# Kernel optimization log

Hardware: AMD Instinct MI355X
Metric: run time of the kernel (lower is better)

## Reference

```python
import jax, jax.numpy as jnp
import numpy as np

SEQ = 2048
D_MODEL = 1024
N_HEADS = 16
TOP_K = 64
Q_LR = 128
KV_LR = 128
ROPE_DIM = 32
V_DIM = 64
IDX_DIM = 64
# Mamba2 indexer block: expand=1, headdim=32, d_state=64, d_conv=4
D_INNER = D_MODEL
M_HD = 32
M_NH = D_INNER // M_HD  # 32 ssm heads
M_DS = 64
M_DC = 4
CONV_CH = D_INNER + 2 * M_DS  # 1152
IN_DIM = 2 * D_INNER + 2 * M_DS + M_NH  # 2208


def _silu(x):
    return x * jax.nn.sigmoid(x)


def _mamba2(x, in_w, conv_w, conv_b, dt_bias, A_log, D, norm_w, out_w):
    # Minimal Mamba2 (SSD) recurrent forward: in_proj -> causal depthwise conv
    # on (x, B, C) -> selective scan with scalar-per-head A -> gated RMSNorm -> out_proj.
    L = x.shape[0]
    zxbcdt = x @ in_w.T  # [L, IN_DIM]
    z = zxbcdt[:, :D_INNER]
    xBC = zxbcdt[:, D_INNER:D_INNER + CONV_CH]
    dt = zxbcdt[:, -M_NH:]
    # causal depthwise conv1d, kernel M_DC
    xp = jnp.pad(xBC, ((M_DC - 1, 0), (0, 0)))
    conv = conv_b
    for k in range(M_DC):
        conv = conv + xp[k:k + L] * conv_w[:, k]
    xBC = _silu(conv)
    xs = xBC[:, :D_INNER].reshape(L, M_NH, M_HD)          # [L,h,p]
    B = xBC[:, D_INNER:D_INNER + M_DS]                     # [L,n]
    C = xBC[:, D_INNER + M_DS:]                            # [L,n]
    dt = jax.nn.softplus(dt + dt_bias)                     # [L,h]
    dA = jnp.exp(dt * (-jnp.exp(A_log)))                   # [L,h]
    dBx = jnp.einsum('lh,lhp,ln->lhpn', dt, xs, B)         # [L,h,p,n]

    def step(h, inp):
        dA_t, dBx_t, C_t = inp
        h = h * dA_t[:, None, None] + dBx_t
        y_t = jnp.einsum('hpn,n->hp', h, C_t)
        return h, y_t

    h0 = jnp.zeros((M_NH, M_HD, M_DS), x.dtype)
    _, y = jax.lax.scan(step, h0, (dA, dBx, C))            # y: [L,h,p]
    y = y + D[:, None] * xs
    y = y.reshape(L, D_INNER) * _silu(z)                   # gated
    y = y * jax.lax.rsqrt(jnp.mean(y * y, axis=-1, keepdims=True) + 1e-5) * norm_w
    return y @ out_w.T


def _make_rope(L):
    inv = 1.0 / (10000.0 ** (jnp.arange(0, ROPE_DIM, 2, dtype=jnp.float32) / ROPE_DIM))
    ang = jnp.arange(L, dtype=jnp.float32)[:, None] * inv  # [L, ROPE/2]
    return jnp.sin(ang), jnp.cos(ang)


def _apply_rope(x, sin, cos):
    # x: [L, H, ROPE_DIM]; rotate-half convention
    x1, x2 = jnp.split(x, 2, axis=-1)
    s = sin[:, None, :]
    c = cos[:, None, :]
    return jnp.concatenate([x1 * c - x2 * s, x1 * s + x2 * c], axis=-1)


def _forward(x, idx_in_w, idx_conv_w, idx_conv_b, idx_dt_bias, idx_A_log, idx_D,
             idx_norm_w, idx_out_w, idx_q_w, idx_k_w, q_down_w, q_up_w, q_rope_w,
             kv_down_w, kv_up_w, k_rope_w, out_w):
    L = x.shape[0]
    # --- Mamba2 indexer scores ---
    x_mamba = _mamba2(x, idx_in_w, idx_conv_w, idx_conv_b, idx_dt_bias,
                      idx_A_log, idx_D, idx_norm_w, idx_out_w)
    q_idx = x_mamba @ idx_q_w.T                            # [L, IDX_DIM]
    k_idx = x @ idx_k_w.T                                  # [L, IDX_DIM]
    scores = (q_idx @ k_idx.T) * (IDX_DIM ** -0.5)         # [L, L]
    mask = jnp.tril(jnp.ones((L, L), dtype=bool))
    scores = jnp.where(mask, scores, -jnp.inf)
    k_val = min(TOP_K, L)
    _, indices = jax.lax.top_k(scores, k_val)              # [L, K]
    # --- MLA low-rank projections ---
    c_q = x @ q_down_w.T                                   # [L, Q_LR]
    q_content = (c_q @ q_up_w.T).reshape(L, N_HEADS, V_DIM)
    q_rope = (c_q @ q_rope_w.T).reshape(L, N_HEADS, ROPE_DIM)
    c_kv = x @ kv_down_w.T                                 # [L, KV_LR]
    kv = c_kv @ kv_up_w.T                                  # [L, 2*H*V]
    k_content_flat, v_flat = jnp.split(kv, 2, axis=-1)
    k_content = k_content_flat.reshape(L, N_HEADS, V_DIM)
    v = v_flat.reshape(L, N_HEADS, V_DIM)
    k_rope_shared = (x @ k_rope_w.T)[:, None, :]           # [L, 1, ROPE]
    sin, cos = _make_rope(L)
    q_rope_rot = _apply_rope(q_rope, sin, cos)
    k_rope_rot = jnp.tile(_apply_rope(k_rope_shared, sin, cos), (1, N_HEADS, 1))
    q_final = jnp.concatenate([q_content, q_rope_rot], axis=-1)  # [L,H,dk]
    k_final = jnp.concatenate([k_content, k_rope_rot], axis=-1)  # [L,H,dk]
    # --- top-k gather sparse attention ---
    k_sparse = k_final[indices]                            # [L,K,H,dk]
    v_sparse = v[indices]                                  # [L,K,H,dv]
    dk = k_final.shape[-1]
    logits = jnp.einsum('lhd,lkhd->lhk', q_final, k_sparse) * (dk ** -0.5)
    w = jax.nn.softmax(logits, axis=-1)
    attn = jnp.einsum('lhk,lkhd->lhd', w, v_sparse).reshape(L, N_HEADS * V_DIM)
    return attn @ out_w.T


def setup_inputs() -> dict:
    key = jax.random.key(0)
    ks = jax.random.split(key, 16)

    def g(k, shape, s=0.02):
        return jax.random.normal(k, shape, jnp.float32) * s

    return {
        "x": jax.random.normal(ks[0], (SEQ, D_MODEL), jnp.float32),
        "idx_in_w": g(ks[1], (IN_DIM, D_MODEL)),
        "idx_conv_w": g(ks[2], (CONV_CH, M_DC), 0.2),
        "idx_conv_b": jnp.zeros((CONV_CH,), jnp.float32),
        "idx_dt_bias": g(ks[3], (M_NH,), 0.1),
        "idx_A_log": jnp.log(jnp.arange(1, M_NH + 1, dtype=jnp.float32)),
        "idx_D": jnp.ones((M_NH,), jnp.float32),
        "idx_norm_w": jnp.ones((D_INNER,), jnp.float32),
        "idx_out_w": g(ks[4], (D_MODEL, D_INNER)),
        "idx_q_w": g(ks[5], (IDX_DIM, D_MODEL)),
        "idx_k_w": g(ks[6], (IDX_DIM, D_MODEL)),
        "q_down_w": g(ks[7], (Q_LR, D_MODEL)),
        "q_up_w": g(ks[8], (N_HEADS * V_DIM, Q_LR)),
        "q_rope_w": g(ks[9], (N_HEADS * ROPE_DIM, Q_LR)),
        "kv_down_w": g(ks[10], (KV_LR, D_MODEL)),
        "kv_up_w": g(ks[11], (2 * N_HEADS * V_DIM, KV_LR)),
        "k_rope_w": g(ks[12], (ROPE_DIM, D_MODEL)),
        "out_w": g(ks[13], (D_MODEL, N_HEADS * V_DIM)),
    }


def reference(x, idx_in_w, idx_conv_w, idx_conv_b, idx_dt_bias, idx_A_log, idx_D,
              idx_norm_w, idx_out_w, idx_q_w, idx_k_w, q_down_w, q_up_w, q_rope_w,
              kv_down_w, kv_up_w, k_rope_w, out_w):
    return _forward(x, idx_in_w, idx_conv_w, idx_conv_b, idx_dt_bias, idx_A_log,
                    idx_D, idx_norm_w, idx_out_w, idx_q_w, idx_k_w, q_down_w,
                    q_up_w, q_rope_w, kv_down_w, kv_up_w, k_rope_w, out_w)
```

## Files before the change

kernel.cpp:

```cpp
#include <hip/hip_runtime.h>
#include <math.h>

constexpr int L      = 2048;
constexpr int NH     = 16;
constexpr int DINNER = 1024;
constexpr int MNH    = 32;
constexpr int CONVCH = 1152;
constexpr int INDIMP = 2304;
constexpr int CHUNK  = 64;
constexpr int NCH    = 32;

using bf16x8 = __attribute__((ext_vector_type(8))) short;
using f32x4  = __attribute__((ext_vector_type(4))) float;

__device__ __forceinline__ f32x4 splat4(float x) { return (f32x4){x, x, x, x}; }

__device__ __forceinline__ unsigned short f2bf(float f) {
  unsigned u = __float_as_uint(f);
  return (unsigned short)((u + 0x7fffu + ((u >> 16) & 1u)) >> 16);
}
__device__ __forceinline__ float bf2f(unsigned short h) {
  return __uint_as_float((unsigned)h << 16);
}

__global__ __launch_bounds__(256) void gemm_f32_v3(
    const float* __restrict__ A, const float* __restrict__ W,
    float* __restrict__ C, int M, int N, int K, int tri) {
  __shared__ float As[16][132];
  __shared__ float Ws[16][132];
  int tid = threadIdx.x;
  int bm = blockIdx.y * 128, bn = blockIdx.x * 128;
  if (tri && bn > bm + 127) return;
  int kper = K / gridDim.z;
  int kb = blockIdx.z * kper, ke = kb + kper;
  int lr = tid >> 1;
  int lh = (tid & 1) * 8;
  int tx = tid & 15, ty = tid >> 4;
  bool wok = (bn + lr < N);
  const float* arow = A + (size_t)(bm + lr) * K + lh;
  const float* wrow = W + (size_t)(bn + lr) * K + lh;
  float4 a0, a1, w0, w1;
  auto gload = [&](int k0) {
    a0 = *(const float4*)(arow + k0);
    a1 = *(const float4*)(arow + k0 + 4);
    w0 = make_float4(0.f, 0.f, 0.f, 0.f); w1 = w0;
    if (wok) {
      w0 = *(const float4*)(wrow + k0);
      w1 = *(const float4*)(wrow + k0 + 4);
    }
  };
  f32x4 acc0[8] = {}, acc1[8] = {};
  gload(kb);
  for (int k0 = kb; k0 < ke; k0 += 16) {
    __syncthreads();
    As[lh+0][lr]=a0.x; As[lh+1][lr]=a0.y; As[lh+2][lr]=a0.z; As[lh+3][lr]=a0.w;
    As[lh+4][lr]=a1.x; As[lh+5][lr]=a1.y; As[lh+6][lr]=a1.z; As[lh+7][lr]=a1.w;
    Ws[lh+0][lr]=w0.x; Ws[lh+1][lr]=w0.y; Ws[lh+2][lr]=w0.z; Ws[lh+3][lr]=w0.w;
    Ws[lh+4][lr]=w1.x; Ws[lh+5][lr]=w1.y; Ws[lh+6][lr]=w1.z; Ws[lh+7][lr]=w1.w;
    __syncthreads();
    if (k0 + 16 < ke) gload(k0 + 16);
#pragma unroll
    for (int kk = 0; kk < 16; ++kk) {
      f32x4 b0 = *(const f32x4*)&Ws[kk][tx * 4];
      f32x4 b1 = *(const f32x4*)&Ws[kk][64 + tx * 4];
      f32x4 al = *(const f32x4*)&As[kk][ty * 8];
      f32x4 ah = *(const f32x4*)&As[kk][ty * 8 + 4];
#pragma unroll
      for (int i = 0; i < 4; ++i) {
        acc0[i]     += splat4(al[i]) * b0;
        acc1[i]     += splat4(al[i]) * b1;
        acc0[i + 4] += splat4(ah[i]) * b0;
        acc1[i + 4] += splat4(ah[i]) * b1;
      }
    }
  }
  bool single = (gridDim.z == 1);
#pragma unroll
  for (int i = 0; i < 8; ++i) {
    int row = bm + ty * 8 + i;
    float* crow = C + (size_t)row * N;
    int c0 = bn + tx * 4, c1 = bn + 64 + tx * 4;
    if (c0 + 3 < N) {
      if (single) *(f32x4*)(crow + c0) = acc0[i];
      else {
        atomicAdd(crow + c0 + 0, acc0[i][0]); atomicAdd(crow + c0 + 1, acc0[i][1]);
        atomicAdd(crow + c0 + 2, acc0[i][2]); atomicAdd(crow + c0 + 3, acc0[i][3]);
      }
    }
    if (c1 + 3 < N) {
      if (single) *(f32x4*)(crow + c1) = acc1[i];
      else {
        atomicAdd(crow + c1 + 0, acc1[i][0]); atomicAdd(crow + c1 + 1, acc1[i][1]);
        atomicAdd(crow + c1 + 2, acc1[i][2]); atomicAdd(crow + c1 + 3, acc1[i][3]);
      }
    }
  }
}

__global__ __launch_bounds__(256) void gemm_f32_dual(
    const float* __restrict__ A0, const float* __restrict__ W0, float* __restrict__ C0,
    const float* __restrict__ A1, const float* __restrict__ W1, float* __restrict__ C1,
    int M, int N, int K, int S) {
  __shared__ float As[16][132];
  __shared__ float Ws[16][132];
  int tid = threadIdx.x;
  int bm = blockIdx.y * 128, bn = blockIdx.x * 128;
  int pair = (int)blockIdx.z >= S;
  int zi = blockIdx.z - pair * S;
  const float* A = pair ? A1 : A0;
  const float* W = pair ? W1 : W0;
  float* C = pair ? C1 : C0;
  int kper = K / S;
  int kb = zi * kper, ke = kb + kper;
  int lr = tid >> 1;
  int lh = (tid & 1) * 8;
  int tx = tid & 15, ty = tid >> 4;
  bool wok = (bn + lr < N);
  const float* arow = A + (size_t)(bm + lr) * K + lh;
  const float* wrow = W + (size_t)(bn + lr) * K + lh;
  float4 a0, a1, w0, w1;
  auto gload = [&](int k0) {
    a0 = *(const float4*)(arow + k0);
    a1 = *(const float4*)(arow + k0 + 4);
    w0 = make_float4(0.f, 0.f, 0.f, 0.f); w1 = w0;
    if (wok) {
      w0 = *(const float4*)(wrow + k0);
      w1 = *(const float4*)(wrow + k0 + 4);
    }
  };
  f32x4 acc0[8] = {}, acc1[8] = {};
  gload(kb);
  for (int k0 = kb; k0 < ke; k0 += 16) {
    __syncthreads();
    As[lh+0][lr]=a0.x; As[lh+1][lr]=a0.y; As[lh+2][lr]=a0.z; As[lh+3][lr]=a0.w;
    As[lh+4][lr]=a1.x; As[lh+5][lr]=a1.y; As[lh+6][lr]=a1.z; As[lh+7][lr]=a1.w;
    Ws[lh+0][lr]=w0.x; Ws[lh+1][lr]=w0.y; Ws[lh+2][lr]=w0.z; Ws[lh+3][lr]=w0.w;
    Ws[lh+4][lr]=w1.x; Ws[lh+5][lr]=w1.y; Ws[lh+6][lr]=w1.z; Ws[lh+7][lr]=w1.w;
    __syncthreads();
    if (k0 + 16 < ke) gload(k0 + 16);
#pragma unroll
    for (int kk = 0; kk < 16; ++kk) {
      f32x4 b0 = *(const f32x4*)&Ws[kk][tx * 4];
      f32x4 b1 = *(const f32x4*)&Ws[kk][64 + tx * 4];
      f32x4 al = *(const f32x4*)&As[kk][ty * 8];
      f32x4 ah = *(const f32x4*)&As[kk][ty * 8 + 4];
#pragma unroll
      for (int i = 0; i < 4; ++i) {
        acc0[i]     += splat4(al[i]) * b0;
        acc1[i]     += splat4(al[i]) * b1;
        acc0[i + 4] += splat4(ah[i]) * b0;
        acc1[i + 4] += splat4(ah[i]) * b1;
      }
    }
  }
#pragma unroll
  for (int i = 0; i < 8; ++i) {
    int row = bm + ty * 8 + i;
    float* crow = C + (size_t)row * N;
    int c0 = bn + tx * 4, c1 = bn + 64 + tx * 4;
    if (c0 + 3 < N) {
      atomicAdd(crow + c0 + 0, acc0[i][0]); atomicAdd(crow + c0 + 1, acc0[i][1]);
      atomicAdd(crow + c0 + 2, acc0[i][2]); atomicAdd(crow + c0 + 3, acc0[i][3]);
    }
    if (c1 + 3 < N) {
      atomicAdd(crow + c1 + 0, acc1[i][0]); atomicAdd(crow + c1 + 1, acc1[i][1]);
      atomicAdd(crow + c1 + 2, acc1[i][2]); atomicAdd(crow + c1 + 3, acc1[i][3]);
    }
  }
}

__global__ __launch_bounds__(256) void gemm_bf16_kernel(
    const unsigned short* __restrict__ A, const unsigned short* __restrict__ W,
    float* __restrict__ C, int M, int N, int K, int lda, int ldb, int ldc) {
  __shared__ unsigned short As[2][128 * 64];
  __shared__ unsigned short Ws[2][128 * 64];
  int tid = threadIdx.x;
  int bx = blockIdx.x, by = blockIdx.y;
  int nxy = gridDim.x * gridDim.y;
  if ((nxy & 7) == 0) {
    int lin = by * gridDim.x + bx;
    int cpx = nxy >> 3;
    int swz = (lin & 7) * cpx + (lin >> 3);
    bx = swz % gridDim.x;
    by = swz / gridDim.x;
  }
  int bm = by * 128, bn = bx * 128;
  int kper = K / gridDim.z;
  int k_begin = blockIdx.z * kper;
  int k_end = k_begin + kper;
  int wv = tid >> 6, lane = tid & 63;
  int wrow = (wv >> 1) * 64, wcol = (wv & 1) * 64;
  int lrow = lane & 15, quad = lane >> 4;

  f32x4 acc[4][4] = {};

  auto stage = [&](int b, int k0) {
#pragma unroll
    for (int it = 0; it < 4; ++it) {
      int s = it * 256 + tid;
      int r = s >> 3;
      int q = (s & 7) ^ (r & 7);
      const unsigned short* ga = A + (size_t)(bm + r) * lda + k0 + q * 8;
      const unsigned short* gw = W + (size_t)(bn + r) * ldb + k0 + q * 8;
      __builtin_amdgcn_global_load_lds((const __attribute__((address_space(1))) void*)ga,
                                       (__attribute__((address_space(3))) void*)&As[b][s * 8], 16, 0, 0);
      __builtin_amdgcn_global_load_lds((const __attribute__((address_space(1))) void*)gw,
                                       (__attribute__((address_space(3))) void*)&Ws[b][s * 8], 16, 0, 0);
    }
  };

  stage(0, k_begin);
  int cur = 0;
  for (int k0 = k_begin; k0 < k_end; k0 += 64) {
    __syncthreads();
    if (k0 + 64 < k_end) stage(cur ^ 1, k0 + 64);
#pragma unroll
    for (int ks = 0; ks < 2; ++ks) {
      bf16x8 af[4], wf[4];
#pragma unroll
      for (int i = 0; i < 4; ++i) {
        int ra = wrow + i * 16 + lrow;
        int qa = (ks * 4 + quad) ^ (ra & 7);
        af[i] = *(const bf16x8*)&As[cur][(ra * 8 + qa) * 8];
        int rw = wcol + i * 16 + lrow;
        int qw = (ks * 4 + quad) ^ (rw & 7);
        wf[i] = *(const bf16x8*)&Ws[cur][(rw * 8 + qw) * 8];
      }
#pragma unroll
      for (int i = 0; i < 4; ++i)
#pragma unroll
        for (int j = 0; j < 4; ++j)
          acc[i][j] = __builtin_amdgcn_mfma_f32_16x16x32_bf16(af[i], wf[j], acc[i][j], 0, 0, 0);
    }
    cur ^= 1;
  }
  bool single = (gridDim.z == 1);
#pragma unroll
  for (int i = 0; i < 4; ++i)
#pragma unroll
    for (int j = 0; j < 4; ++j)
#pragma unroll
      for (int r = 0; r < 4; ++r) {
        int row = bm + wrow + i * 16 + quad * 4 + r;
        int col = bn + wcol + j * 16 + lrow;
        float v = acc[i][j][r];
        if (single) C[(size_t)row * ldc + col] = v;
        else atomicAdd(&C[(size_t)row * ldc + col], v);
      }
}

__global__ __launch_bounds__(512) void gemm_bf16_256_kernel(
    const unsigned short* __restrict__ A, const unsigned short* __restrict__ W,
    float* __restrict__ C, int K, int lda, int ldc) {
  __shared__ unsigned short As[4][256 * 32];
  __shared__ unsigned short Ws[4][256 * 32];
  int tid = threadIdx.x;
  int bx = blockIdx.x, by = blockIdx.y;
  int nxy = gridDim.x * gridDim.y;
  if ((nxy & 7) == 0) {
    int lin = by * gridDim.x + bx;
    int cpx = nxy >> 3;
    int swz = (lin & 7) * cpx + (lin >> 3);
    bx = swz % gridDim.x;
    by = swz / gridDim.x;
  }
  int bm = by * 256, bn = bx * 256;
  int kper = K / gridDim.z;
  int kb = blockIdx.z * kper;
  int U = kper >> 5;
  int wave = tid >> 6, lane = tid & 63;
  int wr = wave >> 2, wc = wave & 3;
  int lrow = lane & 15, quad = lane >> 4;

  f32x4 acc[8][4] = {};

  auto stage = [&](int cell, int u) {
    int k0 = kb + (u << 5);
#pragma unroll
    for (int rd = 0; rd < 2; ++rd) {
      int s = rd * 512 + tid;
      int r = s >> 2;
      int q = (s & 3) ^ ((r >> 1) & 3);
      const unsigned short* ga = A + (size_t)(bm + r) * lda + k0 + q * 8;
      __builtin_amdgcn_global_load_lds((const __attribute__((address_space(1))) void*)ga,
          (__attribute__((address_space(3))) void*)&As[cell][s * 8], 16, 0, 0);
    }
#pragma unroll
    for (int rd = 0; rd < 2; ++rd) {
      int s = rd * 512 + tid;
      int r = s >> 2;
      int q = (s & 3) ^ ((r >> 1) & 3);
      const unsigned short* gw = W + (size_t)(bn + r) * lda + k0 + q * 8;
      __builtin_amdgcn_global_load_lds((const __attribute__((address_space(1))) void*)gw,
          (__attribute__((address_space(3))) void*)&Ws[cell][s * 8], 16, 0, 0);
    }
  };

  auto compute = [&](int cell) {
    bf16x8 af[8], wf[4];
#pragma unroll
    for (int m = 0; m < 8; ++m) {
      int ra = wr * 128 + m * 16 + lrow;
      af[m] = *(const bf16x8*)&As[cell][((ra << 2) + (quad ^ ((ra >> 1) & 3))) * 8];
    }
#pragma unroll
    for (int n = 0; n < 4; ++n) {
      int rw = wc * 64 + n * 16 + lrow;
      wf[n] = *(const bf16x8*)&Ws[cell][((rw << 2) + (quad ^ ((rw >> 1) & 3))) * 8];
    }
    __builtin_amdgcn_s_setprio(1);
#pragma unroll
    for (int m = 0; m < 8; ++m)
#pragma unroll
      for (int n = 0; n < 4; ++n)
        acc[m][n] = __builtin_amdgcn_mfma_f32_16x16x32_bf16(af[m], wf[n], acc[m][n], 0, 0, 0);
    __builtin_amdgcn_s_setprio(0);
  };

  stage(0, 0); stage(1, 1); stage(2, 2);
  for (int u = 0; u + 3 < U; ++u) {
    __builtin_amdgcn_s_barrier();
    asm volatile("" ::: "memory");
    stage((u + 3) & 3, u + 3);
    asm volatile("s_waitcnt vmcnt(12)" ::: "memory");
    __builtin_amdgcn_s_barrier();
    asm volatile("" ::: "memory");
    compute(u & 3);
  }
  for (int u = U - 3; u < U; ++u) {
    __builtin_amdgcn_s_barrier();
    asm volatile("s_waitcnt vmcnt(0)" ::: "memory");
    __builtin_amdgcn_s_barrier();
    asm volatile("" ::: "memory");
    compute(u & 3);
  }

#pragma unroll
  for (int m = 0; m < 8; ++m)
#pragma unroll
    for (int n = 0; n < 4; ++n)
#pragma unroll
      for (int rr = 0; rr < 4; ++rr) {
        int row = bm + wr * 128 + m * 16 + quad * 4 + rr;
        int col = bn + wc * 64 + n * 16 + lrow;
        atomicAdd(&C[(size_t)row * ldc + col], acc[m][n][rr]);
      }
}

__global__ __launch_bounds__(256) void gemm_bf16_dual(
    const unsigned short* __restrict__ A0, const unsigned short* __restrict__ W0,
    float* __restrict__ C0,
    const unsigned short* __restrict__ A1, const unsigned short* __restrict__ W1,
    float* __restrict__ C1,
    int nx0, int ldc0, int ldc1, int K, int ld) {
  __shared__ unsigned short As[2][128 * 64];
  __shared__ unsigned short Ws[2][128 * 64];
  int tid = threadIdx.x;
  int bx = blockIdx.x, by = blockIdx.y;
  int pair = bx >= nx0;
  int bxl = pair ? bx - nx0 : bx;
  const unsigned short* A = pair ? A1 : A0;
  const unsigned short* W = pair ? W1 : W0;
  float* C = pair ? C1 : C0;
  int ldc = pair ? ldc1 : ldc0;
  int bm = by * 128, bn = bxl * 128;
  int wv = tid >> 6, lane = tid & 63;
  int wrow = (wv >> 1) * 64, wcol = (wv & 1) * 64;
  int lrow = lane & 15, quad = lane >> 4;

  f32x4 acc[4][4] = {};

  auto stage = [&](int b, int k0) {
#pragma unroll
    for (int it = 0; it < 4; ++it) {
      int s = it * 256 + tid;
      int r = s >> 3;
      int q = (s & 7) ^ (r & 7);
      const unsigned short* ga = A + (size_t)(bm + r) * ld + k0 + q * 8;
      const unsigned short* gw = W + (size_t)(bn + r) * ld + k0 + q * 8;
      __builtin_amdgcn_global_load_lds((const __attribute__((address_space(1))) void*)ga,
                                       (__attribute__((address_space(3))) void*)&As[b][s * 8], 16, 0, 0);
      __builtin_amdgcn_global_load_lds((const __attribute__((address_space(1))) void*)gw,
                                       (__attribute__((address_space(3))) void*)&Ws[b][s * 8], 16, 0, 0);
    }
  };

  stage(0, 0);
  int cur = 0;
  for (int k0 = 0; k0 < K; k0 += 64) {
    __syncthreads();
    if (k0 + 64 < K) stage(cur ^ 1, k0 + 64);
#pragma unroll
    for (int ks = 0; ks < 2; ++ks) {
      bf16x8 af[4], wf[4];
#pragma unroll
      for (int i = 0; i < 4; ++i) {
        int ra = wrow + i * 16 + lrow;
        int qa = (ks * 4 + quad) ^ (ra & 7);
        af[i] = *(const bf16x8*)&As[cur][(ra * 8 + qa) * 8];
        int rw = wcol + i * 16 + lrow;
        int qw = (ks * 4 + quad) ^ (rw & 7);
        wf[i] = *(const bf16x8*)&Ws[cur][(rw * 8 + qw) * 8];
      }
#pragma unroll
      for (int i = 0; i < 4; ++i)
#pragma unroll
        for (int j = 0; j < 4; ++j)
          acc[i][j] = __builtin_amdgcn_mfma_f32_16x16x32_bf16(af[i], wf[j], acc[i][j], 0, 0, 0);
    }
    cur ^= 1;
  }
#pragma unroll
  for (int i = 0; i < 4; ++i)
#pragma unroll
    for (int j = 0; j < 4; ++j)
#pragma unroll
      for (int r = 0; r < 4; ++r) {
        int row = bm + wrow + i * 16 + quad * 4 + r;
        int col = bn + wcol + j * 16 + lrow;
        C[(size_t)row * ldc + col] = acc[i][j][r];
      }
}

__global__ __launch_bounds__(256) void prep_weights_kernel(
    const float* __restrict__ x, unsigned short* __restrict__ x_trip,
    const float* __restrict__ idx_in_w, unsigned short* __restrict__ w_in_trip,
    const float* __restrict__ q_down_w, const float* __restrict__ kv_down_w,
    const float* __restrict__ k_rope_w, unsigned short* __restrict__ w3down,
    const float* __restrict__ q_up_w, const float* __restrict__ q_rope_w,
    unsigned short* __restrict__ wqups,
    const float* __restrict__ kv_up_w, unsigned short* __restrict__ wkvup,
    const float* __restrict__ idx_out_w, float* __restrict__ out_w_T,
    const float* __restrict__ idx_q_w, float* __restrict__ qwpad,
    float* __restrict__ zxbcdt) {
  __shared__ float tsh[32][33];
  int bid = blockIdx.x;
  if (bid >= 22784) {
    int j = (bid - 22784) * 256 + threadIdx.x;
    zxbcdt[j] = 0.f;
    return;
  }
  if (bid >= 21760) {
    int j = (bid - 21760) * 256 + threadIdx.x;
    qwpad[j] = (j < 65536) ? idx_q_w[j] : 0.f;
    return;
  }
  if (bid >= 20736) {
    int b = bid - 20736;
    int bx = b & 31, by = b >> 5;
    int tx = threadIdx.x & 31, ty8 = threadIdx.x >> 5;
    for (int r = ty8; r < 32; r += 8)
      tsh[r][tx] = idx_out_w[(size_t)(by * 32 + r) * 1024 + bx * 32 + tx];
    __syncthreads();
    for (int r = ty8; r < 32; r += 8)
      out_w_T[(size_t)(bx * 32 + r) * 1024 + by * 32 + tx] = tsh[tx][r];
    return;
  }
  int i = bid * 256 + threadIdx.x;
  if (i < 2097152) {
    float f = x[i];
    unsigned short h = f2bf(f);
    float r1 = f - bf2f(h);
    unsigned short m = f2bf(r1);
    unsigned short l = f2bf(r1 - bf2f(m));
    size_t o = (size_t)i * 6;
    x_trip[o] = h; x_trip[o + 1] = m; x_trip[o + 2] = l;
    x_trip[o + 3] = h; x_trip[o + 4] = m; x_trip[o + 5] = h;
  } else if (i < 4456448) {
    int j = i - 2097152;
    int n = j >> 10, k = j & 1023;
    unsigned short h = 0, m = 0, l = 0;
    if (n < 2208) {
      float f = idx_in_w[(size_t)n * 1024 + k];
      h = f2bf(f);
      float r1 = f - bf2f(h);
      m = f2bf(r1);
      l = f2bf(r1 - bf2f(m));
    }
    size_t o = (size_t)j * 6;
    w_in_trip[o] = h; w_in_trip[o + 1] = h; w_in_trip[o + 2] = h;
    w_in_trip[o + 3] = m; w_in_trip[o + 4] = m; w_in_trip[o + 5] = l;
  } else {
    int j2 = i - 4456448;
    const float* src; unsigned short* dst; int rows, K; size_t obase; int idx;
    if (j2 < 393216) {
      int r = j2 >> 17;
      idx = j2 & 131071;
      K = 1024;
      src = (r == 0) ? q_down_w : (r == 1) ? kv_down_w : k_rope_w;
      rows = (r == 2) ? 32 : 128;
      dst = w3down; obase = (size_t)(r * 131072 + idx) * 3;
    } else if (j2 < 524288) {
      idx = j2 - 393216; K = 128; src = q_up_w; rows = 1024;
      dst = wqups; obase = (size_t)idx * 3;
    } else if (j2 < 589824) {
      idx = j2 - 524288; K = 128; src = q_rope_w; rows = 512;
      dst = wqups; obase = (size_t)393216 + (size_t)idx * 3;
    } else {
      idx = j2 - 589824; K = 128; src = kv_up_w; rows = 2048;
      dst = wkvup; obase = (size_t)idx * 3;
    }
    int n = idx / K, k = idx - n * K;
    unsigned short hi = 0, lo = 0;
    if (n < rows) {
      float f = src[(size_t)n * K + k];
      hi = f2bf(f);
      lo = f2bf(f - bf2f(hi));
    }
    dst[obase] = hi; dst[obase + 1] = hi; dst[obase + 2] = lo;
  }
}

__global__ __launch_bounds__(256) void post_inproj_kernel(
    const float* __restrict__ out_w, unsigned short* __restrict__ w_outp,
    const float* __restrict__ zxbcdt, const float* __restrict__ conv_w,
    const float* __restrict__ conv_b, float* __restrict__ xBC,
    const float* __restrict__ dt_bias, const float* __restrict__ A_log,
    float* __restrict__ dt, float* __restrict__ logdA) {
  int i = blockIdx.x * 256 + threadIdx.x;
  if (i < 1048576) {
    float f = out_w[i];
    unsigned short hi = f2bf(f);
    unsigned short lo = f2bf(f - bf2f(hi));
    size_t o = (size_t)i * 3;
    w_outp[o] = hi; w_outp[o + 1] = hi; w_outp[o + 2] = lo;
  } else if (i < 3407872) {
    int idx = i - 1048576;
    int l = idx / CONVCH, c = idx - l * CONVCH;
    float acc = conv_b[c];
#pragma unroll
    for (int k = 0; k < 4; ++k) {
      int ls = l - 3 + k;
      if (ls >= 0) acc += zxbcdt[(size_t)ls * INDIMP + DINNER + c] * conv_w[c * 4 + k];
    }
    xBC[idx] = acc / (1.f + expf(-acc));
  } else {
    int idx = i - 3407872;
    int l = idx >> 5, h = idx & 31;
    float xv = zxbcdt[(size_t)l * INDIMP + 2176 + h] + dt_bias[h];
    float sp = fmaxf(xv, 0.f) + log1pf(expf(-fabsf(xv)));
    dt[idx] = sp;
    logdA[idx] = sp * -expf(A_log[h]);
  }
}

__global__ __launch_bounds__(256) void conv_augA2_kernel(
    const float* __restrict__ c3, unsigned short* __restrict__ dq,
    unsigned short* __restrict__ dkv) {
  int i = blockIdx.x * 256 + threadIdx.x;
  if (i >= 2048 * 256) return;
  int m = i >> 8, k = i & 255;
  float f = c3[(size_t)m * 384 + k];
  unsigned short hi = f2bf(f);
  unsigned short lo = f2bf(f - bf2f(hi));
  if (k < 128) {
    size_t o = ((size_t)m * 128 + k) * 3;
    dq[o] = hi; dq[o + 1] = lo; dq[o + 2] = hi;
  } else {
    size_t o = ((size_t)m * 128 + (k - 128)) * 3;
    dkv[o] = hi; dkv[o + 1] = lo; dkv[o + 2] = hi;
  }
}

__global__ __launch_bounds__(256) void chunk_G_kernel(
    const float* __restrict__ xBC, float* __restrict__ G,
    const float* __restrict__ logdA, float* __restrict__ lcd) {
  int c = blockIdx.x, tid = threadIdx.x;
  if (c >= NCH) {
    int i = (c - NCH) * 256 + tid;
    int cc = i >> 5, h = i & 31;
    float s = 0.f;
    for (int t = 0; t < CHUNK; ++t) {
      s += logdA[(cc * CHUNK + t) * MNH + h];
      lcd[(size_t)i * CHUNK + t] = s;
    }
    return;
  }
  __shared__ float BsT[64][68];
  __shared__ float Cs[64][65];
  int t = tid >> 2, q = tid & 3;
  const float* row = xBC + (size_t)(c * 64 + t) * CONVCH + DINNER;
#pragma unroll
  for (int j = 0; j < 16; j += 4) {
    float4 b = *(const float4*)(row + q * 16 + j);
    BsT[q * 16 + j + 0][t] = b.x; BsT[q * 16 + j + 1][t] = b.y;
    BsT[q * 16 + j + 2][t] = b.z; BsT[q * 16 + j + 3][t] = b.w;
    float4 cv = *(const float4*)(row + 64 + q * 16 + j);
    Cs[t][q * 16 + j + 0] = cv.x; Cs[t][q * 16 + j + 1] = cv.y;
    Cs[t][q * 16 + j + 2] = cv.z; Cs[t][q * 16 + j + 3] = cv.w;
  }
  __syncthreads();
  int s0 = q * 16;
  f32x4 g0 = {}, g1 = {}, g2 = {}, g3 = {};
  for (int n = 0; n < 64; ++n) {
    f32x4 cv = splat4(Cs[t][n]);
    g0 += cv * *(const f32x4*)&BsT[n][s0];
    g1 += cv * *(const f32x4*)&BsT[n][s0 + 4];
    g2 += cv * *(const f32x4*)&BsT[n][s0 + 8];
    g3 += cv * *(const f32x4*)&BsT[n][s0 + 12];
  }
  float* gp = G + ((size_t)c * 64 + t) * 64 + s0;
  *(f32x4*)gp = g0; *(f32x4*)(gp + 4) = g1; *(f32x4*)(gp + 8) = g2; *(f32x4*)(gp + 12) = g3;
}

__global__ __launch_bounds__(256) void scan_local_kernel(
    const float* __restrict__ xBC, const float* __restrict__ dt,
    const float* __restrict__ lcd, float* __restrict__ hstate) {
  int c = blockIdx.x >> 5, h = blockIdx.x & 31;
  int tid = threadIdx.x;
  __shared__ float Bs[64][68];
  __shared__ float xss[64][36];
  __shared__ float w2s[64];
  int t0 = c * CHUNK;
  int t = tid >> 2, q = tid & 3;
  const float* row = xBC + (size_t)(t0 + t) * CONVCH;
#pragma unroll
  for (int j = 0; j < 16; j += 4)
    *(float4*)&Bs[t][q * 16 + j] = *(const float4*)(row + DINNER + q * 16 + j);
  if (q < 2) {
#pragma unroll
    for (int j = 0; j < 16; j += 4)
      *(float4*)&xss[t][q * 16 + j] = *(const float4*)(row + h * 32 + q * 16 + j);
  }
  if (tid < 64) {
    const float* lc = lcd + ((size_t)c * 32 + h) * CHUNK;
    w2s[tid] = expf(lc[63] - lc[tid]) * dt[(t0 + tid) * MNH + h];
  }
  __syncthreads();
  int n = tid >> 2, pg = (tid & 3) * 8;
  f32x4 h0 = {}, h1 = {};
  for (int s = 0; s < 64; ++s) {
    f32x4 wb = splat4(w2s[s] * Bs[s][n]);
    h0 += wb * *(const f32x4*)&xss[s][pg];
    h1 += wb * *(const f32x4*)&xss[s][pg + 4];
  }
  float* hp = hstate + ((size_t)c * 32 + h) * 2048 + n * 32 + pg;
  *(f32x4*)hp = h0; *(f32x4*)(hp + 4) = h1;
}

__global__ __launch_bounds__(256) void scan_combine_kernel(
    float* __restrict__ hstate, const float* __restrict__ lcd) {
  int i = blockIdx.x * 256 + threadIdx.x;
  int h = i >> 11;
  float H = 0.f;
  for (int c = 0; c < NCH; ++c) {
    float hl = hstate[(size_t)c * 65536 + i];
    hstate[(size_t)c * 65536 + i] = H;
    float P = expf(lcd[((size_t)c * 32 + h) * CHUNK + CHUNK - 1]);
    H = H * P + hl;
  }
}

__global__ __launch_bounds__(256) void scan_y_kernel(
    const float* __restrict__ xBC, const float* __restrict__ G,
    const float* __restrict__ dt, const float* __restrict__ lcd,
    const float* __restrict__ hstate, float* __restrict__ y) {
  int c = blockIdx.x >> 5, h = blockIdx.x & 31;
  int tid = threadIdx.x;
  __shared__ float Ms[64][65];
  __shared__ float Cs[64][65];
  __shared__ float xss[64][36];
  __shared__ float Hss[64][36];
  __shared__ float lcds[64], dts[64];
  int t0 = c * CHUNK;
  int t = tid >> 2, q = tid & 3;
  const float* row = xBC + (size_t)(t0 + t) * CONVCH;
#pragma unroll
  for (int j = 0; j < 16; j += 4) {
    float4 cv = *(const float4*)(row + DINNER + 64 + q * 16 + j);
    Cs[t][q * 16 + j + 0] = cv.x; Cs[t][q * 16 + j + 1] = cv.y;
    Cs[t][q * 16 + j + 2] = cv.z; Cs[t][q * 16 + j + 3] = cv.w;
  }
  if (q < 2) {
#pragma unroll
    for (int j = 0; j < 16; j += 4)
      *(float4*)&xss[t][q * 16 + j] = *(const float4*)(row + h * 32 + q * 16 + j);
  }
  {
    const float* gp = G + ((size_t)c * 64 + t) * 64 + q * 16;
#pragma unroll
    for (int j = 0; j < 16; j += 4) {
      float4 g = *(const float4*)(gp + j);
      Ms[t][q * 16 + j + 0] = g.x; Ms[t][q * 16 + j + 1] = g.y;
      Ms[t][q * 16 + j + 2] = g.z; Ms[t][q * 16 + j + 3] = g.w;
    }
  }
  {
    const float* hp = hstate + ((size_t)c * 32 + h) * 2048 + tid * 8;
    int n = tid >> 2, p0 = (tid & 3) * 8;
    *(float4*)&Hss[n][p0]     = *(const float4*)hp;
    *(float4*)&Hss[n][p0 + 4] = *(const float4*)(hp + 4);
  }
  if (tid < 64) {
    lcds[tid] = lcd[((size_t)c * 32 + h) * CHUNK + tid];
    dts[tid]  = dt[(t0 + tid) * MNH + h];
  }
  __syncthreads();
  {
    int s0 = q * 16;
#pragma unroll
    for (int j = 0; j < 16; ++j) {
      int s = s0 + j;
      float m = (s <= t) ? expf(lcds[t] - lcds[s]) * dts[s] * Ms[t][s] : 0.f;
      Ms[t][s] = m;
    }
  }
  __syncthreads();
  int pg = q * 8;
  f32x4 y0 = {}, y1 = {}, a0 = {}, a1 = {};
  for (int s = 0; s < 64; ++s) {
    f32x4 m = splat4(Ms[t][s]);
    y0 += m * *(const f32x4*)&xss[s][pg];
    y1 += m * *(const f32x4*)&xss[s][pg + 4];
  }
  for (int n = 0; n < 64; ++n) {
    f32x4 cn = splat4(Cs[t][n]);
    a0 += cn * *(const f32x4*)&Hss[n][pg];
    a1 += cn * *(const f32x4*)&Hss[n][pg + 4];
  }
  f32x4 cd = splat4(expf(lcds[t]));
  y0 += cd * a0; y1 += cd * a1;
  float* yp = y + (size_t)(t0 + t) * DINNER + h * 32 + pg;
  *(f32x4*)yp = y0; *(f32x4*)(yp + 4) = y1;
}

__global__ __launch_bounds__(256) void gatenorm_kernel(
    const float* __restrict__ y_ssm, const float* __restrict__ xBC,
    const float* __restrict__ zxbcdt, const float* __restrict__ Dv,
    const float* __restrict__ norm_w, float* __restrict__ out) {
  int l = blockIdx.x, tid = threadIdx.x;
  float vals[4];
  float ss = 0.f;
#pragma unroll
  for (int i = 0; i < 4; ++i) {
    int d = tid + i * 256;
    int h = d >> 5;
    float v = y_ssm[(size_t)l * DINNER + d] + Dv[h] * xBC[(size_t)l * CONVCH + d];
    float z = zxbcdt[(size_t)l * INDIMP + d];
    v *= z / (1.f + expf(-z));
    vals[i] = v;
    ss += v * v;
  }
#pragma unroll
  for (int off = 32; off > 0; off >>= 1) ss += __shfl_xor(ss, off);
  __shared__ float sred[4];
  if ((tid & 63) == 0) sred[tid >> 6] = ss;
  __syncthreads();
  float tot = sred[0] + sred[1] + sred[2] + sred[3];
  float scale = rsqrtf(tot * (1.f / 1024.f) + 1e-5f);
#pragma unroll
  for (int i = 0; i < 4; ++i) {
    int d = tid + i * 256;
    out[(size_t)l * DINNER + d] = vals[i] * scale * norm_w[d];
  }
}

__global__ __launch_bounds__(256) void topk_augA_kernel(
    const float* __restrict__ scores, int* __restrict__ out_idx,
    const float* __restrict__ x, unsigned short* __restrict__ x_aug,
    float* __restrict__ c3) {
  int bid = blockIdx.x, tid = threadIdx.x;
  if (bid >= 10240) {
    int j = (bid - 10240) * 256 + tid;
    c3[j] = 0.f;
    return;
  }
  if (bid >= 2048) {
    int i = (bid - 2048) * 256 + tid;
    float f = x[i];
    unsigned short hi = f2bf(f);
    unsigned short lo = f2bf(f - bf2f(hi));
    size_t o = (size_t)i * 3;
    x_aug[o] = hi; x_aug[o + 1] = lo; x_aug[o + 2] = hi;
    return;
  }
  int l = bid;
  if (l < 64) {
    if (tid < 64) out_idx[l * 64 + tid] = tid;
    return;
  }
  int n = l + 1;
  const float* row = scores + (size_t)l * L;
  __shared__ int hist[256];
  __shared__ unsigned sel_prefix;
  __shared__ int sel_remaining;
  __shared__ int cnt_g, cnt_e;
  __shared__ int eq_list[128];
  if (tid == 0) { cnt_g = 0; cnt_e = 0; }
  unsigned prefix = 0;
  int remaining = 64;
  for (int pass = 0; pass < 4; ++pass) {
    int shift = 24 - 8 * pass;
    unsigned himask = (pass == 0) ? 0u : (0xFFFFFFFFu << (shift + 8));
    hist[tid] = 0;
    __syncthreads();
    for (int j = tid; j < n; j += 256) {
      unsigned u = __float_as_uint(row[j]);
      unsigned key = (u & 0x80000000u) ? ~u : (u | 0x80000000u);
      if (((key ^ prefix) & himask) == 0)
        atomicAdd(&hist[(key >> shift) & 255], 1);
    }
    __syncthreads();
    if (tid == 0) {
      int cum = 0, b = 255;
      for (; b >= 0; --b) {
        cum += hist[b];
        if (cum >= remaining) break;
      }
      sel_prefix = prefix | ((unsigned)b << shift);
      sel_remaining = remaining - (cum - hist[b]);
    }
    __syncthreads();
    prefix = sel_prefix;
    remaining = sel_remaining;
    __syncthreads();
  }
  unsigned T = prefix;
  for (int j = tid; j < n; j += 256) {
    unsigned u = __float_as_uint(row[j]);
    unsigned key = (u & 0x80000000u) ? ~u : (u | 0x80000000u);
    if (key > T) {
      int p = atomicAdd(&cnt_g, 1);
      out_idx[l * 64 + p] = j;
    } else if (key == T) {
      int p = atomicAdd(&cnt_e, 1);
      if (p < 128) eq_list[p] = j;
    }
  }
  __syncthreads();
  if (tid == 0) {
    int G = cnt_g;
    int E = remaining;
    int m = cnt_e < 128 ? cnt_e : 128;
    for (int e = 0; e < E; ++e) {
      int best = 0, bj = 0x7fffffff;
      for (int i = 0; i < m; ++i)
        if (eq_list[i] < bj) { bj = eq_list[i]; best = i; }
      out_idx[l * 64 + G + e] = bj;
      eq_list[best] = 0x7fffffff;
    }
  }
}

__global__ __launch_bounds__(128) void rope_pack_kernel(
    const float* __restrict__ qbuf, const float* __restrict__ kv,
    const float* __restrict__ c3,
    float* __restrict__ q_final, float* __restrict__ k_final) {
  int l = blockIdx.x, tid = threadIdx.x;
  __shared__ float s_s[16], s_c[16];
  if (tid < 16) {
    float inv = powf(10000.f, -(float)tid / 16.f);
    float ang = (float)l * inv;
    s_s[tid] = sinf(ang);
    s_c[tid] = cosf(ang);
  }
  __syncthreads();
  const float* qrow = qbuf + (size_t)l * 1536;
  const float* krow = c3 + (size_t)l * 384 + 256;
  for (int e = tid; e < NH * 96; e += 128) {
    int hh = e / 96, d = e - hh * 96;
    float qv, kvv;
    if (d < 64) {
      qv  = qrow[hh * 64 + d];
      kvv = kv[(size_t)l * 2048 + hh * 64 + d];
    } else {
      int r = d - 64;
      if (r < 16) {
        float q1 = qrow[1024 + hh * 32 + r];
        float q2 = qrow[1024 + hh * 32 + 16 + r];
        qv = q1 * s_c[r] - q2 * s_s[r];
        float k1 = krow[r];
        float k2 = krow[16 + r];
        kvv = k1 * s_c[r] - k2 * s_s[r];
      } else {
        int rr = r - 16;
        float q1 = qrow[1024 + hh * 32 + rr];
        float q2 = qrow[1024 + hh * 32 + 16 + rr];
        qv = q1 * s_s[rr] + q2 * s_c[rr];
        float k1 = krow[rr];
        float k2 = krow[16 + rr];
        kvv = k1 * s_s[rr] + k2 * s_c[rr];
      }
    }
    q_final[(size_t)l * 1536 + e] = qv;
    k_final[(size_t)l * 1536 + e] = kvv;
  }
}

__global__ __launch_bounds__(256) void attn_out_kernel(
    const float* __restrict__ q_final, const float* __restrict__ k_final,
    const float* __restrict__ kv, const int* __restrict__ idx,
    unsigned short* __restrict__ attn_aug, float* __restrict__ outz) {
  int b = blockIdx.x;
  int tid = threadIdx.x;
  if (b >= 2048) {
    int j = (b - 2048) * 256 + tid;
    outz[j] = 0.f;
    return;
  }
  int l = (b & 7) * 256 + (b >> 3);
  int h = tid >> 4;
  int s = tid & 15;
  __shared__ __align__(16) float lg[16][64];
  __shared__ int iks[64];

  if (tid < 64) iks[tid] = idx[l * 64 + tid];

  const float* qrow = q_final + (size_t)l * 1536 + h * 96 + s * 2;
  float q0 = qrow[0],  q1 = qrow[1];
  float q2 = qrow[32], q3 = qrow[33];
  float q4 = qrow[64], q5 = qrow[65];
  __syncthreads();

#pragma unroll 4
  for (int k = 0; k < 64; ++k) {
    const float* kr = k_final + (size_t)iks[k] * 1536 + h * 96 + s * 2;
    float2 a = *(const float2*)kr;
    float2 b2 = *(const float2*)(kr + 32);
    float2 c = *(const float2*)(kr + 64);
    float d = q0 * a.x + q1 * a.y + q2 * b2.x + q3 * b2.y + q4 * c.x + q5 * c.y;
    d += __shfl_xor(d, 1);
    d += __shfl_xor(d, 2);
    d += __shfl_xor(d, 4);
    d += __shfl_xor(d, 8);
    if (s == 0) lg[h][k] = d * 0.10206207261596575f;
  }
  __syncthreads();

  f32x4 lv = *(const f32x4*)&lg[h][s * 4];
  float m = fmaxf(fmaxf(lv[0], lv[1]), fmaxf(lv[2], lv[3]));
#pragma unroll
  for (int off = 1; off < 16; off <<= 1) m = fmaxf(m, __shfl_xor(m, off));
  f32x4 ev;
  ev[0] = expf(lv[0] - m); ev[1] = expf(lv[1] - m);
  ev[2] = expf(lv[2] - m); ev[3] = expf(lv[3] - m);
  float ssum = ev[0] + ev[1] + ev[2] + ev[3];
#pragma unroll
  for (int off = 1; off < 16; off <<= 1) ssum += __shfl_xor(ssum, off);
  float inv = 1.f / ssum;
  lg[h][s * 4 + 0] = ev[0] * inv;
  lg[h][s * 4 + 1] = ev[1] * inv;
  lg[h][s * 4 + 2] = ev[2] * inv;
  lg[h][s * 4 + 3] = ev[3] * inv;
  __syncthreads();

  f32x4 acc = {};
#pragma unroll 4
  for (int k = 0; k < 64; ++k) {
    const float* vr = kv + (size_t)iks[k] * 2048 + 1024 + tid * 4;
    f32x4 v = *(const f32x4*)vr;
    acc += splat4(lg[h][k]) * v;
  }

#pragma unroll
  for (int i = 0; i < 4; ++i) {
    float a = acc[i];
    unsigned short hi = f2bf(a);
    unsigned short lo = f2bf(a - bf2f(hi));
    size_t o = ((size_t)l * 1024 + tid * 4 + i) * 3;
    attn_aug[o] = hi; attn_aug[o + 1] = lo; attn_aug[o + 2] = hi;
  }
}

extern "C" void kernel_launch(void* const* d_in, const int* in_sizes, int n_in,
                              void* d_out, int out_size, void* d_ws, size_t ws_size,
                              hipStream_t stream) {
  const float* x          = (const float*)d_in[0];
  const float* idx_in_w   = (const float*)d_in[1];
  const float* idx_conv_w = (const float*)d_in[2];
  const float* idx_conv_b = (const float*)d_in[3];
  const float* idx_dt_b   = (const float*)d_in[4];
  const float* idx_A_log  = (const float*)d_in[5];
  const float* idx_D      = (const float*)d_in[6];
  const float* idx_norm_w = (const float*)d_in[7];
  const float* idx_out_w  = (const float*)d_in[8];
  const float* idx_q_w    = (const float*)d_in[9];
  const float* idx_k_w    = (const float*)d_in[10];
  const float* q_down_w   = (const float*)d_in[11];
  const float* q_up_w     = (const float*)d_in[12];
  const float* q_rope_w   = (const float*)d_in[13];
  const float* kv_down_w  = (const float*)d_in[14];
  const float* kv_up_w    = (const float*)d_in[15];
  const float* k_rope_w   = (const float*)d_in[16];
  const float* out_w      = (const float*)d_in[17];
  float* out = (float*)d_out;

  float* p = (float*)d_ws;
  float* segA = p; p += 4718592;
  float* segB = p; p += 2359296;
  float* dtb = p; p += 65536;
  float* logdA = p; p += 65536;
  float* lcdb = p; p += 65536;
  int*   idxb = (int*)p; p += 131072;
  float* segD = p; p += 4194304;
  float* segBig1 = p; p += 6291456;
  float* segBig2 = p; p += 7077888;
  float* segH = p; p += 3145728;
  unsigned short* w_3down_aug = (unsigned short*)p; p += 589824;
  unsigned short* w_qups_aug  = (unsigned short*)p; p += 294912;
  unsigned short* w_kvup_aug  = (unsigned short*)p; p += 393216;
  unsigned short* c_q_aug     = (unsigned short*)p; p += 393216;
  unsigned short* c_kv_aug    = (unsigned short*)p; p += 393216;
  float* Gbuf = p; p += 131072;

  float* zxbcdt = segA;
  float* scores = segA;
  float* qbuf   = segA;
  float* xBC    = segB;
  float* q_idx  = segB;
  float* k_idx  = segB + 131072;
  float* c3     = segB + 262144;
  float* y_ssm  = segD;
  float* hstate = segD + 2097152;
  float* kvb    = segD;
  unsigned short* x_trip     = (unsigned short*)segBig1;
  unsigned short* w_outp_aug = (unsigned short*)segBig1;
  unsigned short* w_in_trip  = (unsigned short*)segBig2;
  float* y_norm  = segBig2;
  unsigned short* x_aug = (unsigned short*)segBig2;
  float* q_final = segBig2;
  unsigned short* attn_aug = (unsigned short*)(segBig2 + 3145728);
  float* out_w_T = segH;
  float* qwpad   = segH + 1048576;
  float* Wq      = segH + 1179648;
  float* k_final = segH;

  dim3 blk(256);
  auto cdiv = [](int a, int b) { return (a + b - 1) / b; };
  auto gemmf3 = [&](const float* A, const float* W, float* C, int M, int N, int K, int S, int tri) {
    dim3 grid(cdiv(N, 128), M / 128, S);
    hipLaunchKernelGGL(gemm_f32_v3, grid, blk, 0, stream, A, W, C, M, N, K, tri);
  };
  auto gemmb = [&](const unsigned short* A, const unsigned short* W, float* C,
                   int M, int N, int K, int lda, int ldb, int ldc, int S) {
    dim3 grid(N / 128, M / 128, S);
    hipLaunchKernelGGL(gemm_bf16_kernel, grid, blk, 0, stream, A, W, C, M, N, K, lda, ldb, ldc);
  };

  hipLaunchKernelGGL(prep_weights_kernel, dim3(41216), blk, 0, stream,
                     x, x_trip, idx_in_w, w_in_trip,
                     q_down_w, kv_down_w, k_rope_w, w_3down_aug,
                     q_up_w, q_rope_w, w_qups_aug, kv_up_w, w_kvup_aug,
                     idx_out_w, out_w_T, idx_q_w, qwpad, zxbcdt);
  gemmf3(qwpad, out_w_T, Wq, 128, 1024, 1024, 8, 0);

  {
    dim3 grid(9, 8, 3);
    hipLaunchKernelGGL(gemm_bf16_256_kernel, grid, dim3(512), 0, stream,
                       x_trip, w_in_trip, zxbcdt, 6144, 6144, INDIMP);
  }
  hipLaunchKernelGGL(post_inproj_kernel, dim3(13568), blk, 0, stream,
                     out_w, w_outp_aug, zxbcdt, idx_conv_w, idx_conv_b, xBC,
                     idx_dt_b, idx_A_log, dtb, logdA);
  hipLaunchKernelGGL(chunk_G_kernel, dim3(NCH + 4), blk, 0, stream,
                     xBC, Gbuf, logdA, lcdb);
  hipLaunchKernelGGL(scan_local_kernel, dim3(NCH * MNH), blk, 0, stream,
                     xBC, dtb, lcdb, hstate);
  hipLaunchKernelGGL(scan_combine_kernel, dim3(256), blk, 0, stream, hstate, lcdb);
  hipLaunchKernelGGL(scan_y_kernel, dim3(NCH * MNH), blk, 0, stream,
                     xBC, Gbuf, dtb, lcdb, hstate, y_ssm);
  hipLaunchKernelGGL(gatenorm_kernel, dim3(L), blk, 0, stream,
                     y_ssm, xBC, zxbcdt, idx_D, idx_norm_w, y_norm);

  hipMemsetAsync(q_idx, 0, 262144 * 4, stream);
  {
    dim3 grid(1, 16, 32);
    hipLaunchKernelGGL(gemm_f32_dual, grid, blk, 0, stream,
                       y_norm, Wq, q_idx, x, idx_k_w, k_idx, 2048, 64, 1024, 16);
  }
  gemmf3(q_idx, k_idx, scores, 2048, 2048, 64, 1, 1);
  hipLaunchKernelGGL(topk_augA_kernel, dim3(13312), blk, 0, stream,
                     scores, idxb, x, x_aug, c3);

  gemmb(x_aug, w_3down_aug, c3, 2048, 384, 3072, 3072, 3072, 384, 8);
  hipLaunchKernelGGL(conv_augA2_kernel, dim3(cdiv(2048 * 256, 256)), blk, 0, stream,
                     c3, c_q_aug, c_kv_aug);
  {
    dim3 grid(28, 16, 1);
    hipLaunchKernelGGL(gemm_bf16_dual, grid, blk, 0, stream,
                       c_q_aug, w_qups_aug, qbuf,
                       c_kv_aug, w_kvup_aug, kvb,
                       12, 1536, 2048, 384, 384);
  }
  hipLaunchKernelGGL(rope_pack_kernel, dim3(L), dim3(128), 0, stream,
                     qbuf, kvb, c3, q_final, k_final);

  hipLaunchKernelGGL(attn_out_kernel, dim3(10240), blk, 0, stream,
                     q_final, k_final, kvb, idxb, attn_aug, out);
  gemmb(attn_aug, w_outp_aug, out, 2048, 1024, 3072, 3072, 3072, 1024, 4);
}
```

Measured before the change: 625.7 us.

## Fuse chunk cumsum into post-inproj, merge G and local scan, use 256-tile out GEMM

The per-chunk log-decay cumulative sum now runs as extra blocks of post_inproj_kernel, computed straight from zxbcdt, so the intermediate logdA buffer goes away. The chunk Gram (G) computation and the local state scan are merged into one kernel launch that shares a single shared-memory array, removing a launch and a serialization point. The final output projection switches from the 128-tile split-K bf16 GEMM to the 256-tile kernel with a 6-way split. This cuts launches and memory traffic but relies on the 256-tile kernel's split semantics and atomic or accumulating output matching the old path.

```diff
diff --git a/kernel.cpp b/kernel.cpp
--- a/kernel.cpp
+++ b/kernel.cpp
@@ -516,8 +516,25 @@
     const float* __restrict__ zxbcdt, const float* __restrict__ conv_w,
     const float* __restrict__ conv_b, float* __restrict__ xBC,
     const float* __restrict__ dt_bias, const float* __restrict__ A_log,
-    float* __restrict__ dt, float* __restrict__ logdA) {
-  int i = blockIdx.x * 256 + threadIdx.x;
+    float* __restrict__ dt, float* __restrict__ lcd) {
+  int bid = blockIdx.x;
+  if (bid >= 13568) {
+    int i = (bid - 13568) * 256 + threadIdx.x;
+    int c = i >> 5, h = i & 31;
+    float bias = dt_bias[h];
+    float nega = -expf(A_log[h]);
+    float s = 0.f;
+    const float* zp = zxbcdt + (size_t)(c * CHUNK) * INDIMP + 2176 + h;
+    float* lp = lcd + (size_t)i * CHUNK;
+    for (int t = 0; t < CHUNK; ++t) {
+      float xv = zp[(size_t)t * INDIMP] + bias;
+      float sp = fmaxf(xv, 0.f) + log1pf(expf(-fabsf(xv)));
+      s += sp * nega;
+      lp[t] = s;
+    }
+    return;
+  }
+  int i = bid * 256 + threadIdx.x;
   if (i < 1048576) {
     float f = out_w[i];
     unsigned short hi = f2bf(f);
@@ -540,7 +557,6 @@
     float xv = zxbcdt[(size_t)l * INDIMP + 2176 + h] + dt_bias[h];
     float sp = fmaxf(xv, 0.f) + log1pf(expf(-fabsf(xv)));
     dt[idx] = sp;
-    logdA[idx] = sp * -expf(A_log[h]);
   }
 }
 
@@ -562,55 +578,46 @@
   }
 }
 
-__global__ __launch_bounds__(256) void chunk_G_kernel(
+__global__ __launch_bounds__(256) void chunkG_scanA_kernel(
     const float* __restrict__ xBC, float* __restrict__ G,
-    const float* __restrict__ logdA, float* __restrict__ lcd) {
-  int c = blockIdx.x, tid = threadIdx.x;
-  if (c >= NCH) {
-    int i = (c - NCH) * 256 + tid;
-    int cc = i >> 5, h = i & 31;
-    float s = 0.f;
-    for (int t = 0; t < CHUNK; ++t) {
-      s += logdA[(cc * CHUNK + t) * MNH + h];
-      lcd[(size_t)i * CHUNK + t] = s;
-    }
+    const float* __restrict__ dt, const float* __restrict__ lcd,
+    float* __restrict__ hstate) {
+  __shared__ float sh[64 * 68 + 64 * 65];
+  int bid = blockIdx.x, tid = threadIdx.x;
+  if (bid < NCH) {
+    int c = bid;
+    float (*BsT)[68] = (float(*)[68])sh;
+    float (*Cs)[65]  = (float(*)[65])(sh + 64 * 68);
+    int t = tid >> 2, q = tid & 3;
+    const float* row = xBC + (size_t)(c * 64 + t) * CONVCH + DINNER;
+#pragma unroll
+    for (int j = 0; j < 16; j += 4) {
+      float4 b = *(const float4*)(row + q * 16 + j);
+      BsT[q * 16 + j + 0][t] = b.x; BsT[q * 16 + j + 1][t] = b.y;
+      BsT[q * 16 + j + 2][t] = b.z; BsT[q * 16 + j + 3][t] = b.w;
+      float4 cv = *(const float4*)(row + 64 + q * 16 + j);
+      Cs[t][q * 16 + j + 0] = cv.x; Cs[t][q * 16 + j + 1] = cv.y;
+      Cs[t][q * 16 + j + 2] = cv.z; Cs[t][q * 16 + j + 3] = cv.w;
+    }
+    __syncthreads();
+    int s0 = q * 16;
+    f32x4 g0 = {}, g1 = {}, g2 = {}, g3 = {};
+    for (int n = 0; n < 64; ++n) {
+      f32x4 cv = splat4(Cs[t][n]);
+      g0 += cv * *(const f32x4*)&BsT[n][s0];
+      g1 += cv * *(const f32x4*)&BsT[n][s0 + 4];
+      g2 += cv * *(const f32x4*)&BsT[n][s0 + 8];
+      g3 += cv * *(const f32x4*)&BsT[n][s0 + 12];
+    }
+    float* gp = G + ((size_t)c * 64 + t) * 64 + s0;
+    *(f32x4*)gp = g0; *(f32x4*)(gp + 4) = g1; *(f32x4*)(gp + 8) = g2; *(f32x4*)(gp + 12) = g3;
     return;
   }
-  __shared__ float BsT[64][68];
-  __shared__ float Cs[64][65];
-  int t = tid >> 2, q = tid & 3;
-  const float* row = xBC + (size_t)(c * 64 + t) * CONVCH + DINNER;
-#pragma unroll
-  for (int j = 0; j < 16; j += 4) {
-    float4 b = *(const float4*)(row + q * 16 + j);
-    BsT[q * 16 + j + 0][t] = b.x; BsT[q * 16 + j + 1][t] = b.y;
-    BsT[q * 16 + j + 2][t] = b.z; BsT[q * 16 + j + 3][t] = b.w;
-    float4 cv = *(const float4*)(row + 64 + q * 16 + j);
-    Cs[t][q * 16 + j + 0] = cv.x; Cs[t][q * 16 + j + 1] = cv.y;
-    Cs[t][q * 16 + j + 2] = cv.z; Cs[t][q * 16 + j + 3] = cv.w;
-  }
-  __syncthreads();
-  int s0 = q * 16;
-  f32x4 g0 = {}, g1 = {}, g2 = {}, g3 = {};
-  for (int n = 0; n < 64; ++n) {
-    f32x4 cv = splat4(Cs[t][n]);
-    g0 += cv * *(const f32x4*)&BsT[n][s0];
-    g1 += cv * *(const f32x4*)&BsT[n][s0 + 4];
-    g2 += cv * *(const f32x4*)&BsT[n][s0 + 8];
-    g3 += cv * *(const f32x4*)&BsT[n][s0 + 12];
-  }
-  float* gp = G + ((size_t)c * 64 + t) * 64 + s0;
-  *(f32x4*)gp = g0; *(f32x4*)(gp + 4) = g1; *(f32x4*)(gp + 8) = g2; *(f32x4*)(gp + 12) = g3;
-}
-
-__global__ __launch_bounds__(256) void scan_local_kernel(
-    const float* __restrict__ xBC, const float* __restrict__ dt,
-    const float* __restrict__ lcd, float* __restrict__ hstate) {
-  int c = blockIdx.x >> 5, h = blockIdx.x & 31;
-  int tid = threadIdx.x;
-  __shared__ float Bs[64][68];
-  __shared__ float xss[64][36];
-  __shared__ float w2s[64];
+  int b2 = bid - NCH;
+  int c = b2 >> 5, h = b2 & 31;
+  float (*Bs)[68]  = (float(*)[68])sh;
+  float (*xss)[36] = (float(*)[36])(sh + 64 * 68);
+  float* w2s = sh + 64 * 68 + 64 * 36;
   int t0 = c * CHUNK;
   int t = tid >> 2, q = tid & 3;
   const float* row = xBC + (size_t)(t0 + t) * CONVCH;
@@ -1002,6 +1009,7 @@
   unsigned short* c_q_aug     = (unsigned short*)p; p += 393216;
   unsigned short* c_kv_aug    = (unsigned short*)p; p += 393216;
   float* Gbuf = p; p += 131072;
+  (void)logdA;
 
   float* zxbcdt = segA;
   float* scores = segA;
@@ -1049,13 +1057,11 @@
     hipLaunchKernelGGL(gemm_bf16_256_kernel, grid, dim3(512), 0, stream,
                        x_trip, w_in_trip, zxbcdt, 6144, 6144, INDIMP);
   }
-  hipLaunchKernelGGL(post_inproj_kernel, dim3(13568), blk, 0, stream,
+  hipLaunchKernelGGL(post_inproj_kernel, dim3(13572), blk, 0, stream,
                      out_w, w_outp_aug, zxbcdt, idx_conv_w, idx_conv_b, xBC,
-                     idx_dt_b, idx_A_log, dtb, logdA);
-  hipLaunchKernelGGL(chunk_G_kernel, dim3(NCH + 4), blk, 0, stream,
-                     xBC, Gbuf, logdA, lcdb);
-  hipLaunchKernelGGL(scan_local_kernel, dim3(NCH * MNH), blk, 0, stream,
-                     xBC, dtb, lcdb, hstate);
+                     idx_dt_b, idx_A_log, dtb, lcdb);
+  hipLaunchKernelGGL(chunkG_scanA_kernel, dim3(NCH + NCH * MNH), blk, 0, stream,
+                     xBC, Gbuf, dtb, lcdb, hstate);
   hipLaunchKernelGGL(scan_combine_kernel, dim3(256), blk, 0, stream, hstate, lcdb);
   hipLaunchKernelGGL(scan_y_kernel, dim3(NCH * MNH), blk, 0, stream,
                      xBC, Gbuf, dtb, lcdb, hstate, y_ssm);
@@ -1087,5 +1093,9 @@
 
   hipLaunchKernelGGL(attn_out_kernel, dim3(10240), blk, 0, stream,
                      q_final, k_final, kvb, idxb, attn_aug, out);
-  gemmb(attn_aug, w_outp_aug, out, 2048, 1024, 3072, 3072, 3072, 1024, 4);
-}
+  {
+    dim3 grid(4, 8, 6);
+    hipLaunchKernelGGL(gemm_bf16_256_kernel, grid, dim3(512), 0, stream,
+                       attn_aug, w_outp_aug, out, 3072, 3072, 1024);
+  }
+}
```

Result: slower. 676.3 us (+8.1%).
